# Optimization experiments

Measured on AMD Instinct MI355X. Metric: run time of the kernel, lower is better.

Reference implementation:

```python
import jax, jax.numpy as jnp
import numpy as np

EMBED = 1024
HEADS = 16
HEAD_DIM = EMBED // HEADS
FFN = 4096
BSZ = 2
CHUNK = 128
NCHUNK = 16
REG_LEN = CHUNK * NCHUNK   # 2048
SUM_LEN = NCHUNK           # 1 summary token per chunk
NEG = -1e9


def _layer_norm(x, g, b, eps=1e-5):
    mu = x.mean(-1, keepdims=True)
    var = ((x - mu) ** 2).mean(-1, keepdims=True)
    return (x - mu) * jax.lax.rsqrt(var + eps) * g + b


def _build_mask(reg_chunk_ranges, sum_len, reg_len):
    # True = attention allowed. Museformer hierarchical scheme:
    #   rr: reg token attends reg tokens of its OWN chunk, causally
    #   rs: reg token attends summary tokens of STRICTLY EARLIER chunks
    #   sr: summary token of chunk c attends reg tokens of chunk c
    #   ss: causal among summary tokens
    bsz = reg_chunk_ranges.shape[0]
    starts = reg_chunk_ranges[:, :, 0]                       # [B, C]
    t = jnp.arange(reg_len)
    chunk_id = (t[None, :, None] >= starts[:, None, :]).sum(-1) - 1   # [B, R]
    sum_chunk = jnp.arange(sum_len)                          # [S]
    rr = (chunk_id[:, :, None] == chunk_id[:, None, :]) & (t[None, :, None] >= t[None, None, :])
    rs = sum_chunk[None, None, :] < chunk_id[:, :, None]     # [B, R, S]
    sr = chunk_id[:, None, :] == sum_chunk[None, :, None]    # [B, S, R]
    ss = jnp.broadcast_to(sum_chunk[:, None] >= sum_chunk[None, :], (bsz, sum_len, sum_len))
    top = jnp.concatenate([ss, sr], axis=2)
    bot = jnp.concatenate([rs, rr], axis=2)
    return jnp.concatenate([top, bot], axis=1)               # [B, S+R, S+R]


def _forward(x, w_q, w_k, w_v, w_o,
             ln_sa_sum_g, ln_sa_sum_b, ln_sa_reg_g, ln_sa_reg_b,
             sum_fc1_w, sum_fc1_b, sum_fc2_w, sum_fc2_b,
             reg_fc1_w, reg_fc1_b, reg_fc2_w, reg_fc2_b,
             ln_f_sum_g, ln_f_sum_b, ln_f_reg_g, ln_f_reg_b,
             reg_chunk_ranges, sum_len, reg_len):
    bsz, total, d = x.shape
    # --- self-attention block (pre-norm, separate LN for sum/reg parts) ---
    hs = _layer_norm(x[:, :sum_len], ln_sa_sum_g, ln_sa_sum_b)
    hr = _layer_norm(x[:, sum_len:], ln_sa_reg_g, ln_sa_reg_b)
    h = jnp.concatenate([hs, hr], axis=1)
    q = (h @ w_q.T).reshape(bsz, total, HEADS, HEAD_DIM)
    k = (h @ w_k.T).reshape(bsz, total, HEADS, HEAD_DIM)
    v = (h @ w_v.T).reshape(bsz, total, HEADS, HEAD_DIM)
    scores = jnp.einsum('bqhd,bkhd->bhqk', q, k) * (HEAD_DIM ** -0.5)
    mask = _build_mask(reg_chunk_ranges, sum_len, reg_len)   # [B, T, T] bool
    scores = jnp.where(mask[:, None], scores, NEG)
    attn = jax.nn.softmax(scores, axis=-1)
    ctx = jnp.einsum('bhqk,bkhd->bqhd', attn, v).reshape(bsz, total, d)
    x = x + ctx @ w_o.T
    # --- FFN block (pre-norm, separate LN/FFN for sum/reg parts) ---
    fs = _layer_norm(x[:, :sum_len], ln_f_sum_g, ln_f_sum_b)
    fs = jax.nn.relu(fs @ sum_fc1_w.T + sum_fc1_b) @ sum_fc2_w.T + sum_fc2_b
    fr = _layer_norm(x[:, sum_len:], ln_f_reg_g, ln_f_reg_b)
    fr = jax.nn.relu(fr @ reg_fc1_w.T + reg_fc1_b) @ reg_fc2_w.T + reg_fc2_b
    return x + jnp.concatenate([fs, fr], axis=1)


def setup_inputs() -> dict:
    key = jax.random.key(0)
    ks = jax.random.split(key, 12)
    s = 0.02
    total = SUM_LEN + REG_LEN
    starts = (np.arange(NCHUNK) * CHUNK).astype(np.int32)
    ranges = np.stack([starts, starts + CHUNK], axis=-1)     # [C, 2]
    reg_chunk_ranges = jnp.asarray(np.broadcast_to(ranges, (BSZ, NCHUNK, 2)).copy())
    d = dict(
        x=jax.random.normal(ks[0], (BSZ, total, EMBED), jnp.float32),
        w_q=jax.random.normal(ks[1], (EMBED, EMBED), jnp.float32) * s,
        w_k=jax.random.normal(ks[2], (EMBED, EMBED), jnp.float32) * s,
        w_v=jax.random.normal(ks[3], (EMBED, EMBED), jnp.float32) * s,
        w_o=jax.random.normal(ks[4], (EMBED, EMBED), jnp.float32) * s,
        ln_sa_sum_g=jnp.ones((EMBED,)), ln_sa_sum_b=jnp.zeros((EMBED,)),
        ln_sa_reg_g=jnp.ones((EMBED,)), ln_sa_reg_b=jnp.zeros((EMBED,)),
        sum_fc1_w=jax.random.normal(ks[5], (FFN, EMBED), jnp.float32) * s,
        sum_fc1_b=jnp.zeros((FFN,)),
        sum_fc2_w=jax.random.normal(ks[6], (EMBED, FFN), jnp.float32) * s,
        sum_fc2_b=jnp.zeros((EMBED,)),
        reg_fc1_w=jax.random.normal(ks[7], (FFN, EMBED), jnp.float32) * s,
        reg_fc1_b=jnp.zeros((FFN,)),
        reg_fc2_w=jax.random.normal(ks[8], (EMBED, FFN), jnp.float32) * s,
        reg_fc2_b=jnp.zeros((EMBED,)),
        ln_f_sum_g=jnp.ones((EMBED,)), ln_f_sum_b=jnp.zeros((EMBED,)),
        ln_f_reg_g=jnp.ones((EMBED,)), ln_f_reg_b=jnp.zeros((EMBED,)),
        reg_chunk_ranges=reg_chunk_ranges,
        sum_len=SUM_LEN,
        reg_len=REG_LEN,
    )
    return d


def reference(x, w_q, w_k, w_v, w_o,
              ln_sa_sum_g, ln_sa_sum_b, ln_sa_reg_g, ln_sa_reg_b,
              sum_fc1_w, sum_fc1_b, sum_fc2_w, sum_fc2_b,
              reg_fc1_w, reg_fc1_b, reg_fc2_w, reg_fc2_b,
              ln_f_sum_g, ln_f_sum_b, ln_f_reg_g, ln_f_reg_b,
              reg_chunk_ranges, sum_len, reg_len):
    return _forward(x, w_q, w_k, w_v, w_o,
                    ln_sa_sum_g, ln_sa_sum_b, ln_sa_reg_g, ln_sa_reg_b,
                    sum_fc1_w, sum_fc1_b, sum_fc2_w, sum_fc2_b,
                    reg_fc1_w, reg_fc1_b, reg_fc2_w, reg_fc2_b,
                    ln_f_sum_g, ln_f_sum_b, ln_f_reg_g, ln_f_reg_b,
                    reg_chunk_ranges, sum_len, reg_len)
```

## Files before the change

### kernel.cpp

```cpp
#include <hip/hip_runtime.h>
#include <stdint.h>

typedef __attribute__((ext_vector_type(8))) short short8;
typedef __attribute__((ext_vector_type(4))) float f32x4;

__device__ __forceinline__ float bf2f(short s) {
    union { unsigned u; float f; } c;
    c.u = ((unsigned)(unsigned short)s) << 16;
    return c.f;
}
__device__ __forceinline__ short f2bf(float f) {
    union { float f; unsigned u; } c; c.f = f;
    unsigned u = c.u + 0x7fffu + ((c.u >> 16) & 1u);
    return (short)(u >> 16);
}
__device__ __forceinline__ void gll16(const short* g, short* l) {
    __builtin_amdgcn_global_load_lds(
        (const __attribute__((address_space(1))) unsigned int*)g,
        (__attribute__((address_space(3))) unsigned int*)l, 16, 0, 0);
}
#define MFMA(a, b, c) __builtin_amdgcn_mfma_f32_16x16x32_bf16((a), (b), (c), 0, 0, 0)

__global__ __launch_bounds__(256) void cvt_w(
    const float* __restrict__ wq, const float* __restrict__ wk,
    const float* __restrict__ wv, const float* __restrict__ wo,
    const float* __restrict__ f1s, const float* __restrict__ f2s,
    const float* __restrict__ f1r, const float* __restrict__ f2r,
    short* __restrict__ dst)
{
    size_t i = ((size_t)blockIdx.x * 256 + threadIdx.x) * 4;
    const float* src; size_t off;
    if (i < 4194304) {
        int seg = (int)(i >> 20);
        src = seg == 0 ? wq : seg == 1 ? wk : seg == 2 ? wv : wo;
        off = i & 1048575;
    } else {
        size_t ii = i - 4194304;
        int seg = (int)(ii >> 22);
        src = seg == 0 ? f1s : seg == 1 ? f2s : seg == 2 ? f1r : f2r;
        off = ii & 4194303;
    }
    float4 v = *(const float4*)(src + off);
    short4 o;
    o.x = f2bf(v.x); o.y = f2bf(v.y); o.z = f2bf(v.z); o.w = f2bf(v.w);
    *(short4*)(dst + i) = o;
}

template<int PHASE>
__global__ __launch_bounds__(256) void ln_k(
    const float* __restrict__ xin, const short* __restrict__ Pw, float* __restrict__ x1out,
    const float* __restrict__ g_sum, const float* __restrict__ b_sum,
    const float* __restrict__ g_reg, const float* __restrict__ b_reg,
    short* __restrict__ out_all, short* __restrict__ out_s, short* __restrict__ out_r)
{
    int row = blockIdx.x;
    int b = row / 2064, t = row - b * 2064;
    int tid = threadIdx.x;
    int c = tid * 4;
    size_t base = (size_t)row * 1024 + c;
    float4 v = *(const float4*)(xin + base);
    if (PHASE == 1) {
#pragma unroll
        for (int z = 0; z < 2; ++z) {
            short4 p = *(const short4*)(Pw + (size_t)z * 4227072 + base);
            v.x += bf2f(p.x); v.y += bf2f(p.y);
            v.z += bf2f(p.z); v.w += bf2f(p.w);
        }
        *(float4*)(x1out + base) = v;
    }
    float s = v.x + v.y + v.z + v.w;
#pragma unroll
    for (int off = 1; off < 64; off <<= 1) s += __shfl_xor(s, off);
    __shared__ float red[8];
    if ((tid & 63) == 0) red[tid >> 6] = s;
    __syncthreads();
    float mu = (red[0] + red[1] + red[2] + red[3]) * (1.0f / 1024.0f);
    float a0 = v.x - mu, a1 = v.y - mu, a2 = v.z - mu, a3 = v.w - mu;
    float qq = a0 * a0 + a1 * a1 + a2 * a2 + a3 * a3;
#pragma unroll
    for (int off = 1; off < 64; off <<= 1) qq += __shfl_xor(qq, off);
    if ((tid & 63) == 0) red[4 + (tid >> 6)] = qq;
    __syncthreads();
    float var = (red[4] + red[5] + red[6] + red[7]) * (1.0f / 1024.0f);
    float rs = rsqrtf(var + 1e-5f);
    const float* g  = (t < 16) ? g_sum : g_reg;
    const float* be = (t < 16) ? b_sum : b_reg;
    short4 o;
    o.x = f2bf(a0 * rs * g[c]     + be[c]);
    o.y = f2bf(a1 * rs * g[c + 1] + be[c + 1]);
    o.z = f2bf(a2 * rs * g[c + 2] + be[c + 2]);
    o.w = f2bf(a3 * rs * g[c + 3] + be[c + 3]);
    short* dst;
    if (PHASE == 0) dst = out_all + (size_t)row * 1024;
    else dst = (t < 16) ? (out_s + ((size_t)b * 16 + t) * 1024)
                        : (out_r + ((size_t)b * 2048 + (t - 16)) * 1024);
    *(short4*)(dst + c) = o;
}

template<int MODE>
__global__ __launch_bounds__(512, 2) void gemm8p(
    const short* __restrict__ A, int M, int K, int klen,
    const short* __restrict__ B0, const short* __restrict__ B1, const short* __restrict__ B2,
    const float* __restrict__ bias,
    void* __restrict__ o0, void* __restrict__ o1, void* __restrict__ o2, int seg)
{
    const int tid = threadIdx.x;
    const int w = tid >> 6, l = tid & 63;
    const int lr = l & 15, lh = l >> 4;
    const int m0 = blockIdx.x * 256;
    int ntile = blockIdx.y, nsel = 0;
    const short* B = B0;
    if (MODE == 0) { nsel = ntile >> 2; ntile &= 3; B = nsel == 0 ? B0 : (nsel == 1 ? B1 : B2); }
    const int n0 = ntile * 256;
    const int wm = w >> 2, wn = w & 3;
    const int kbase = blockIdx.z * klen;

    __shared__ __align__(16) short L[2 * 32768];

    const int srow = tid >> 2;
    const int scb  = (tid & 3) ^ ((srow >> 1) & 3);
    int ar0 = m0 + srow;        if (ar0 > M - 1) ar0 = M - 1;
    int ar1 = m0 + srow + 128;  if (ar1 > M - 1) ar1 = M - 1;
    const short* gA0 = A + (size_t)ar0 * K + kbase + scb * 8;
    const short* gA1 = A + (size_t)ar1 * K + kbase + scb * 8;
    const short* gB0 = B + (size_t)(n0 + srow) * K + kbase + scb * 8;
    const short* gB1 = B + (size_t)(n0 + srow + 128) * K + kbase + scb * 8;
    const int wofs = w * 512;
    const int cbrd = (lh ^ ((lr >> 1) & 3)) * 8;

    f32x4 acc[8][4];
#pragma unroll
    for (int m = 0; m < 8; ++m)
#pragma unroll
        for (int n = 0; n < 4; ++n) acc[m][n] = (f32x4){0.f, 0.f, 0.f, 0.f};

    auto STG = [&](int tt, int s, bool isB) {
        const int off = (tt & 1) * 32768 + s * 16384 + (isB ? 8192 : 0);
        const int gk  = tt * 64 + s * 32;
        if (!isB) {
            gll16(gA0 + gk, L + off + wofs);
            gll16(gA1 + gk, L + off + 4096 + wofs);
        } else {
            gll16(gB0 + gk, L + off + wofs);
            gll16(gB1 + gk, L + off + 4096 + wofs);
        }
    };

    const int nt = klen >> 6;
    STG(0, 0, false); STG(0, 0, true); STG(0, 1, false); STG(0, 1, true);

    const int arow = wm * 128, brow = wn * 64;

    for (int t = 0; t < nt; ++t) {
        const int buf = (t & 1) * 32768;
        const short* LA0 = L + buf;
        const short* LB0 = L + buf + 8192;
        const short* LA1 = L + buf + 16384;
        const short* LB1 = L + buf + 24576;

        asm volatile("s_waitcnt vmcnt(4)" ::: "memory");
        __builtin_amdgcn_s_barrier();
        asm volatile("" ::: "memory");
        if (t + 1 < nt) STG(t + 1, 0, false);
        short8 a0[8];
#pragma unroll
        for (int m = 0; m < 8; ++m)
            a0[m] = *(const short8*)(LA0 + (arow + m * 16 + lr) * 32 + cbrd);
        short8 b0 = *(const short8*)(LB0 + (brow + lr) * 32 + cbrd);
        short8 b1 = *(const short8*)(LB0 + (brow + 16 + lr) * 32 + cbrd);
        __builtin_amdgcn_s_setprio(1);
#pragma unroll
        for (int m = 0; m < 8; ++m) {
            acc[m][0] = MFMA(a0[m], b0, acc[m][0]);
            acc[m][1] = MFMA(a0[m], b1, acc[m][1]);
        }
        __builtin_amdgcn_s_setprio(0);

        if (t + 1 < nt) asm volatile("s_waitcnt vmcnt(2)" ::: "memory");
        else            asm volatile("s_waitcnt vmcnt(0)" ::: "memory");
        __builtin_amdgcn_s_barrier();
        asm volatile("" ::: "memory");
        if (t + 1 < nt) STG(t + 1, 0, true);
        short8 b2 = *(const short8*)(LB0 + (brow + 32 + lr) * 32 + cbrd);
        short8 b3 = *(const short8*)(LB0 + (brow + 48 + lr) * 32 + cbrd);
        __builtin_amdgcn_s_setprio(1);
#pragma unroll
        for (int m = 0; m < 8; ++m) {
            acc[m][2] = MFMA(a0[m], b2, acc[m][2]);
            acc[m][3] = MFMA(a0[m], b3, acc[m][3]);
        }
        __builtin_amdgcn_s_setprio(0);
        short8 a1[8];
#pragma unroll
        for (int m = 0; m < 8; ++m)
            a1[m] = *(const short8*)(LA1 + (arow + m * 16 + lr) * 32 + cbrd);
        short8 c0 = *(const short8*)(LB1 + (brow + lr) * 32 + cbrd);
        short8 c1 = *(const short8*)(LB1 + (brow + 16 + lr) * 32 + cbrd);

        __builtin_amdgcn_s_barrier();
        asm volatile("" ::: "memory");
        if (t + 1 < nt) STG(t + 1, 1, false);
        __builtin_amdgcn_s_setprio(1);
#pragma unroll
        for (int m = 0; m < 8; ++m) {
            acc[m][0] = MFMA(a1[m], c0, acc[m][0]);
            acc[m][1] = MFMA(a1[m], c1, acc[m][1]);
        }
        __builtin_amdgcn_s_setprio(0);
        short8 c2 = *(const short8*)(LB1 + (brow + 32 + lr) * 32 + cbrd);
        short8 c3 = *(const short8*)(LB1 + (brow + 48 + lr) * 32 + cbrd);

        __builtin_amdgcn_s_barrier();
        asm volatile("" ::: "memory");
        if (t + 1 < nt) STG(t + 1, 1, true);
        __builtin_amdgcn_s_setprio(1);
#pragma unroll
        for (int m = 0; m < 8; ++m) {
            acc[m][2] = MFMA(a1[m], c2, acc[m][2]);
            acc[m][3] = MFMA(a1[m], c3, acc[m][3]);
        }
        __builtin_amdgcn_s_setprio(0);
    }

#pragma unroll
    for (int m = 0; m < 8; ++m) {
#pragma unroll
        for (int n = 0; n < 4; ++n) {
            int gc = n0 + wn * 64 + n * 16 + lr;
#pragma unroll
            for (int j = 0; j < 4; ++j) {
                int gr = m0 + wm * 128 + m * 16 + lh * 4 + j;
                if (gr >= M) continue;
                float val = acc[m][n][j];
                if (MODE == 0) {
                    short* o = (short*)(nsel == 0 ? o0 : (nsel == 1 ? o1 : o2));
                    o[(size_t)gr * 1024 + gc] = f2bf(val);
                } else if (MODE == 2) {
                    val += bias[gc];
                    val = val > 0.f ? val : 0.f;
                    ((short*)o0)[(size_t)gr * 4096 + gc] = f2bf(val);
                } else {
                    short* P = (short*)o0 + (size_t)blockIdx.z * (size_t)seg;
                    P[(size_t)gr * 1024 + gc] = f2bf(val);
                }
            }
        }
    }
}

template<int MODE>
__global__ __launch_bounds__(256) void gemm_bt(
    const short* __restrict__ A, int M, int K, int klen,
    const short* __restrict__ B0,
    const float* __restrict__ bias,
    void* __restrict__ o0, int seg)
{
    const int tid = threadIdx.x;
    const int w = tid >> 6, l = tid & 63;
    const int lr = l & 15, lh = l >> 4;
    const int m0 = blockIdx.x * 128;
    const int n0 = blockIdx.y * 128;
    const short* B = B0;
    const int wr = (w >> 1) * 64, wc = (w & 1) * 64;
    const int kbase = blockIdx.z * klen;

    __shared__ __align__(16) short As[2 * 4096];
    __shared__ __align__(16) short Bs[2 * 4096];

    const int srow = w * 32 + (l >> 2);
    const int scol = (((l & 3) ^ ((l >> 3) & 3))) * 8;
    int ar0 = m0 + srow;      if (ar0 > M - 1) ar0 = M - 1;
    int ar1 = m0 + srow + 16; if (ar1 > M - 1) ar1 = M - 1;
    const short* ga0 = A + (size_t)ar0 * K + scol + kbase;
    const short* ga1 = A + (size_t)ar1 * K + scol + kbase;
    const short* gb0 = B + (size_t)(n0 + srow) * K + scol + kbase;
    const short* gb1 = B + (size_t)(n0 + srow + 16) * K + scol + kbase;
    const int lofs = (w * 32) * 32;
    const int cbrd = (lh ^ ((lr >> 1) & 3)) * 8;

    f32x4 acc[4][4];
#pragma unroll
    for (int m = 0; m < 4; ++m)
#pragma unroll
        for (int n = 0; n < 4; ++n) acc[m][n] = (f32x4){0.f, 0.f, 0.f, 0.f};

    auto STAGE = [&](int j, int buf) {
        const int k0 = j * 32;
        short* a = As + buf * 4096 + lofs;
        short* b = Bs + buf * 4096 + lofs;
        gll16(ga0 + k0, a);
        gll16(ga1 + k0, a + 512);
        gll16(gb0 + k0, b);
        gll16(gb1 + k0, b + 512);
    };

    const int nk = klen >> 5;
    STAGE(0, 0);
    for (int t = 0; t < nk; ++t) {
        __syncthreads();
        const int cur = (t & 1);
        if (t + 1 < nk) STAGE(t + 1, cur ^ 1);
        const int co = cur << 12;
        short8 af[4], bfr[4];
#pragma unroll
        for (int m = 0; m < 4; ++m)
            af[m] = *(const short8*)(As + co + (wr + m * 16 + lr) * 32 + cbrd);
#pragma unroll
        for (int n = 0; n < 4; ++n)
            bfr[n] = *(const short8*)(Bs + co + (wc + n * 16 + lr) * 32 + cbrd);
#pragma unroll
        for (int m = 0; m < 4; ++m)
#pragma unroll
            for (int n = 0; n < 4; ++n)
                acc[m][n] = MFMA(af[m], bfr[n], acc[m][n]);
    }

#pragma unroll
    for (int m = 0; m < 4; ++m) {
#pragma unroll
        for (int n = 0; n < 4; ++n) {
            int gc = n0 + wc + n * 16 + lr;
#pragma unroll
            for (int j = 0; j < 4; ++j) {
                int gr = m0 + wr + m * 16 + lh * 4 + j;
                if (gr >= M) continue;
                float val = acc[m][n][j];
                if (MODE == 1) {
                    float* P = (float*)o0 + (size_t)blockIdx.z * (size_t)seg;
                    P[(size_t)gr * 1024 + gc] = val;
                } else {
                    val += bias[gc];
                    val = val > 0.f ? val : 0.f;
                    ((short*)o0)[(size_t)gr * 4096 + gc] = f2bf(val);
                }
            }
        }
    }
}

__global__ __launch_bounds__(256) void reduce_f2reg(
    const float* __restrict__ x1, const short* __restrict__ P,
    const float* __restrict__ bias, float* __restrict__ out)
{
    size_t i = ((size_t)blockIdx.x * 256 + threadIdx.x) * 4;
    int gr = (int)(i >> 10), c = (int)(i & 1023);
    size_t g = (size_t)((gr >> 11) * 2064 + 16 + (gr & 2047)) * 1024 + c;
    float4 r  = *(const float4*)(x1 + g);
    float4 bb = *(const float4*)(bias + c);
    float ox = r.x + bb.x, oy = r.y + bb.y, oz = r.z + bb.z, ow = r.w + bb.w;
#pragma unroll
    for (int z = 0; z < 4; ++z) {
        short4 p = *(const short4*)(P + (size_t)z * 4194304 + i);
        ox += bf2f(p.x); oy += bf2f(p.y); oz += bf2f(p.z); ow += bf2f(p.w);
    }
    float4 o; o.x = ox; o.y = oy; o.z = oz; o.w = ow;
    *(float4*)(out + g) = o;
}

__global__ __launch_bounds__(256) void reduce_f2sum(
    const float* __restrict__ x1, const float* __restrict__ P,
    const float* __restrict__ bias, float* __restrict__ out)
{
    int i = (blockIdx.x * 256 + threadIdx.x) * 4;
    int gr = i >> 10, c = i & 1023;
    size_t g = (size_t)((gr >> 4) * 2064 + (gr & 15)) * 1024 + c;
    float4 r  = *(const float4*)(x1 + g);
    float4 bb = *(const float4*)(bias + c);
    float ox = r.x + bb.x, oy = r.y + bb.y, oz = r.z + bb.z, ow = r.w + bb.w;
#pragma unroll
    for (int s = 0; s < 16; ++s) {
        float4 p = *(const float4*)(P + s * 32768 + i);
        ox += p.x; oy += p.y; oz += p.z; ow += p.w;
    }
    float4 o; o.x = ox; o.y = oy; o.z = oz; o.w = ow;
    *(float4*)(out + g) = o;
}

__global__ __launch_bounds__(256) void attn_reg(
    const short* __restrict__ q, const short* __restrict__ k,
    const short* __restrict__ v, short* __restrict__ ctx)
{
    __shared__ __align__(16) short Pl[128 * 168];
    __shared__ __align__(16) short Vt[64 * 168];
    short* Kl = Pl;

    const int tid = threadIdx.x;
    const int w = tid >> 6, l = tid & 63, lr = l & 15, lh = l >> 4;
    const int c = blockIdx.x, h = blockIdx.y, b = blockIdx.z;
    const int hc = h * 64;
    const size_t rowq0 = (size_t)b * 2064 + 16 + (size_t)c * 128;

    for (int ch = tid; ch < 1152; ch += 256) {
        int row = ch >> 3, kk = (ch & 7) << 3;
        size_t grow = (row < 16) ? ((size_t)b * 2064 + row) : (rowq0 + row - 16);
        *(int4*)(Kl + row * 72 + kk) = *(const int4*)(k + grow * 1024 + hc + kk);
    }
    for (int ch = tid; ch < 1152; ch += 256) {
        int j = ch % 144, db = ch / 144;
        size_t grow = (j < 16) ? ((size_t)b * 2064 + j) : (rowq0 + j - 16);
        short8 dv = *(const short8*)(v + grow * 1024 + hc + db * 8);
#pragma unroll
        for (int i = 0; i < 8; ++i) Vt[(db * 8 + i) * 168 + j] = dv[i];
    }
    for (int idx = tid; idx < 1024; idx += 256) {
        int d = idx >> 4, jj = 144 + (idx & 15);
        Vt[d * 168 + jj] = 0;
    }
    __syncthreads();

    short8 qf[2][2];
#pragma unroll
    for (int m = 0; m < 2; ++m) {
        size_t grow = rowq0 + w * 32 + m * 16 + lr;
#pragma unroll
        for (int ks = 0; ks < 2; ++ks)
            qf[m][ks] = *(const short8*)(q + grow * 1024 + hc + ks * 32 + lh * 8);
    }

    f32x4 s[2][9];
#pragma unroll
    for (int m = 0; m < 2; ++m)
#pragma unroll
        for (int n = 0; n < 9; ++n) s[m][n] = (f32x4){0.f, 0.f, 0.f, 0.f};
    __builtin_amdgcn_s_setprio(1);
#pragma unroll
    for (int n = 0; n < 9; ++n) {
        const short* kr = Kl + (n * 16 + lr) * 72;
        short8 k0 = *(const short8*)(kr + lh * 8);
        short8 k1 = *(const short8*)(kr + 32 + lh * 8);
        s[0][n] = MFMA(qf[0][0], k0, s[0][n]);
        s[0][n] = MFMA(qf[0][1], k1, s[0][n]);
        s[1][n] = MFMA(qf[1][0], k0, s[1][n]);
        s[1][n] = MFMA(qf[1][1], k1, s[1][n]);
    }
    __builtin_amdgcn_s_setprio(0);

    float inv_[2][4];
#pragma unroll
    for (int m = 0; m < 2; ++m) {
#pragma unroll
        for (int j = 0; j < 4; ++j) {
            int p = w * 32 + m * 16 + lh * 4 + j;
            float best = -1e30f;
            float e[9];
#pragma unroll
            for (int n = 0; n < 9; ++n) {
                int kk = n * 16 + lr;
                bool vis = (kk < 16) ? (kk < c) : (kk - 16 <= p);
                float val = vis ? s[m][n][j] * 0.125f : -1e30f;
                e[n] = val;
                best = fmaxf(best, val);
            }
#pragma unroll
            for (int off = 1; off < 16; off <<= 1) best = fmaxf(best, __shfl_xor(best, off));
            float sm = 0.f;
#pragma unroll
            for (int n = 0; n < 9; ++n) {
                float ex = __expf(e[n] - best);
                s[m][n][j] = ex;
                sm += ex;
            }
#pragma unroll
            for (int off = 1; off < 16; off <<= 1) sm += __shfl_xor(sm, off);
            inv_[m][j] = 1.0f / sm;
        }
    }

    __syncthreads();
#pragma unroll
    for (int m = 0; m < 2; ++m)
#pragma unroll
        for (int n = 0; n < 9; ++n)
#pragma unroll
            for (int j = 0; j < 4; ++j)
                Pl[(w * 32 + m * 16 + lh * 4 + j) * 168 + n * 16 + lr] = f2bf(s[m][n][j]);
    for (int idx = l; idx < 512; idx += 64) {
        int rr = idx >> 4, kkp = 144 + (idx & 15);
        Pl[(w * 32 + rr) * 168 + kkp] = 0;
    }
    __syncthreads();

    f32x4 dacc[2][4];
#pragma unroll
    for (int m = 0; m < 2; ++m)
#pragma unroll
        for (int n = 0; n < 4; ++n) dacc[m][n] = (f32x4){0.f, 0.f, 0.f, 0.f};
#pragma unroll
    for (int ks = 0; ks < 5; ++ks) {
        int kk0 = ks * 32;
        short8 pa[2];
#pragma unroll
        for (int m = 0; m < 2; ++m)
            pa[m] = *(const short8*)(Pl + (w * 32 + m * 16 + lr) * 168 + kk0 + lh * 8);
        __builtin_amdgcn_s_setprio(1);
#pragma unroll
        for (int n = 0; n < 4; ++n) {
            short8 vb = *(const short8*)(Vt + (n * 16 + lr) * 168 + kk0 + lh * 8);
            dacc[0][n] = MFMA(pa[0], vb, dacc[0][n]);
            dacc[1][n] = MFMA(pa[1], vb, dacc[1][n]);
        }
        __builtin_amdgcn_s_setprio(0);
    }

#pragma unroll
    for (int m = 0; m < 2; ++m)
#pragma unroll
        for (int n = 0; n < 4; ++n)
#pragma unroll
            for (int j = 0; j < 4; ++j) {
                int p = w * 32 + m * 16 + lh * 4 + j;
                ctx[(rowq0 + p) * 1024 + hc + n * 16 + lr] = f2bf(dacc[m][n][j] * inv_[m][j]);
            }
}

__global__ __launch_bounds__(64) void attn_sum(
    const short* __restrict__ q, const short* __restrict__ k,
    const short* __restrict__ v, short* __restrict__ ctx)
{
    int idx = blockIdx.x;
    int b = idx >> 8, h = (idx >> 4) & 15, s = idx & 15;
    int l = threadIdx.x;
    int hc = h * 64;
    size_t qrow = (size_t)b * 2064 + s;
    __shared__ float qv[64];
    __shared__ float pp[192];
    qv[l] = bf2f(q[qrow * 1024 + hc + l]);
    __syncthreads();
    float sc[3];
#pragma unroll
    for (int i = 0; i < 3; ++i) {
        int j = l + i * 64;
        float t = -1e30f;
        if (j < 144 && (j >= 16 || j <= s)) {
            size_t kr = (j < 16) ? ((size_t)b * 2064 + j)
                                 : ((size_t)b * 2064 + 16 + (size_t)s * 128 + (j - 16));
            const short* kp = k + kr * 1024 + hc;
            float acc = 0.f;
            for (int d = 0; d < 64; ++d) acc += qv[d] * bf2f(kp[d]);
            t = acc * 0.125f;
        }
        sc[i] = t;
    }
    float mx = fmaxf(sc[0], fmaxf(sc[1], sc[2]));
#pragma unroll
    for (int off = 1; off < 64; off <<= 1) mx = fmaxf(mx, __shfl_xor(mx, off));
    float sm = 0.f;
#pragma unroll
    for (int i = 0; i < 3; ++i) {
        float ex = (sc[i] > -1e29f) ? __expf(sc[i] - mx) : 0.f;
        pp[l + i * 64] = ex;
        sm += ex;
    }
#pragma unroll
    for (int off = 1; off < 64; off <<= 1) sm += __shfl_xor(sm, off);
    __syncthreads();
    float invs = 1.0f / sm;
    float acc = 0.f;
    for (int j = 0; j < 144; ++j) {
        float pj = pp[j];
        size_t vr = (j < 16) ? ((size_t)b * 2064 + j)
                             : ((size_t)b * 2064 + 16 + (size_t)s * 128 + (j - 16));
        acc += pj * bf2f(v[vr * 1024 + hc + l]);
    }
    ctx[qrow * 1024 + hc + l] = f2bf(acc * invs);
}

extern "C" void kernel_launch(void* const* d_in, const int* in_sizes, int n_in,
                              void* d_out, int out_size, void* d_ws, size_t ws_size,
                              hipStream_t stream) {
    const float* x    = (const float*)d_in[0];
    const float* wq   = (const float*)d_in[1];
    const float* wk   = (const float*)d_in[2];
    const float* wv   = (const float*)d_in[3];
    const float* wo   = (const float*)d_in[4];
    const float* lsg  = (const float*)d_in[5];
    const float* lsb  = (const float*)d_in[6];
    const float* lrg  = (const float*)d_in[7];
    const float* lrb  = (const float*)d_in[8];
    const float* sf1w = (const float*)d_in[9];
    const float* sf1b = (const float*)d_in[10];
    const float* sf2w = (const float*)d_in[11];
    const float* sf2b = (const float*)d_in[12];
    const float* rf1w = (const float*)d_in[13];
    const float* rf1b = (const float*)d_in[14];
    const float* rf2w = (const float*)d_in[15];
    const float* rf2b = (const float*)d_in[16];
    const float* fsg  = (const float*)d_in[17];
    const float* fsb  = (const float*)d_in[18];
    const float* frg  = (const float*)d_in[19];
    const float* frb  = (const float*)d_in[20];
    float* out = (float*)d_out;

    char* ws = (char*)d_ws;
    short* wbf   = (short*)ws;
    short* wq_b  = wbf;
    short* wk_b  = wbf + 1048576;
    short* wv_b  = wbf + 2097152;
    short* wo_b  = wbf + 3145728;
    short* f1s_b = wbf + 4194304;
    short* f2s_b = wbf + 8388608;
    short* f1r_b = wbf + 12582912;
    short* f2r_b = wbf + 16777216;
    short* h_all = (short*)(ws + 41943040);
    short* qb   = (short*)(ws + 50397184);
    short* kb   = qb + 4227072;
    short* vb   = kb + 4227072;
    short* ctxb = vb + 4227072;
    short* Pwo  = (short*)(ws + 41943040);
    float* x1   = (float*)(ws + 84213760);
    short* h2_reg = (short*)ws;
    short* h2_sum = (short*)(ws + 75759616);
    short* f1_reg = (short*)(ws + 41943040);
    short* f1_sum = (short*)(ws + 75825152);
    float* Psum   = (float*)(ws + 8388608);
    short* Pf2    = (short*)ws;

    cvt_w<<<20480, 256, 0, stream>>>(wq, wk, wv, wo, sf1w, sf2w, rf1w, rf2w, wbf);
    ln_k<0><<<4128, 256, 0, stream>>>(x, nullptr, nullptr, lsg, lsb, lrg, lrb,
                                      h_all, nullptr, nullptr);
    gemm8p<0><<<dim3(17, 12, 1), 512, 0, stream>>>(h_all, 4128, 1024, 1024,
        wq_b, wk_b, wv_b, nullptr, qb, kb, vb, 0);
    attn_reg<<<dim3(16, 16, 2), 256, 0, stream>>>(qb, kb, vb, ctxb);
    attn_sum<<<512, 64, 0, stream>>>(qb, kb, vb, ctxb);
    gemm8p<3><<<dim3(17, 4, 2), 512, 0, stream>>>(ctxb, 4128, 1024, 512,
        wo_b, nullptr, nullptr, nullptr, Pwo, nullptr, nullptr, 4227072);
    ln_k<1><<<4128, 256, 0, stream>>>(x, Pwo, x1, fsg, fsb, frg, frb,
                                      nullptr, h2_sum, h2_reg);
    gemm8p<2><<<dim3(16, 16, 1), 512, 0, stream>>>(h2_reg, 4096, 1024, 1024,
        f1r_b, nullptr, nullptr, rf1b, f1_reg, nullptr, nullptr, 0);
    gemm_bt<2><<<dim3(1, 32, 1), 256, 0, stream>>>(h2_sum, 32, 1024, 1024,
        f1s_b, sf1b, f1_sum, 0);
    gemm_bt<1><<<dim3(1, 8, 16), 256, 0, stream>>>(f1_sum, 32, 4096, 256,
        f2s_b, nullptr, Psum, 32768);
    reduce_f2sum<<<32, 256, 0, stream>>>(x1, Psum, sf2b, out);
    gemm8p<3><<<dim3(16, 4, 4), 512, 0, stream>>>(f1_reg, 4096, 4096, 1024,
        f2r_b, nullptr, nullptr, nullptr, Pf2, nullptr, nullptr, 4194304);
    reduce_f2reg<<<4096, 256, 0, stream>>>(x1, Pf2, rf2b, out);
}
```

Before: 277.2 us.

## Add 256x128-tile GEMM variant for QKV and output projections

Result: slower. 290.2 us (+4.7%).

```diff
diff --git a/kernel.cpp b/kernel.cpp
--- a/kernel.cpp
+++ b/kernel.cpp
@@ -239,6 +239,151 @@
                     val += bias[gc];
                     val = val > 0.f ? val : 0.f;
                     ((short*)o0)[(size_t)gr * 4096 + gc] = f2bf(val);
+                } else {
+                    short* P = (short*)o0 + (size_t)blockIdx.z * (size_t)seg;
+                    P[(size_t)gr * 1024 + gc] = f2bf(val);
+                }
+            }
+        }
+    }
+}
+
+template<int MODE>
+__global__ __launch_bounds__(512, 2) void gemm4q(
+    const short* __restrict__ A, int M, int K, int klen,
+    const short* __restrict__ B0, const short* __restrict__ B1, const short* __restrict__ B2,
+    void* __restrict__ o0, void* __restrict__ o1, void* __restrict__ o2, int seg)
+{
+    const int tid = threadIdx.x;
+    const int w = tid >> 6, l = tid & 63;
+    const int lr = l & 15, lh = l >> 4;
+    const int m0 = blockIdx.x * 256;
+    int ntile = blockIdx.y, nsel = 0;
+    const short* B = B0;
+    if (MODE == 0) { nsel = ntile >> 3; ntile &= 7; B = nsel == 0 ? B0 : (nsel == 1 ? B1 : B2); }
+    const int n0 = ntile * 128;
+    const int wm = w >> 1, wn = w & 1;
+    const int kbase = blockIdx.z * klen;
+
+    __shared__ __align__(16) short L[2 * 24576];
+
+    const int srow = tid >> 2;
+    const int scb  = (tid & 3) ^ ((srow >> 1) & 3);
+    int ar0 = m0 + srow;        if (ar0 > M - 1) ar0 = M - 1;
+    int ar1 = m0 + srow + 128;  if (ar1 > M - 1) ar1 = M - 1;
+    const short* gA0 = A + (size_t)ar0 * K + kbase + scb * 8;
+    const short* gA1 = A + (size_t)ar1 * K + kbase + scb * 8;
+    const short* gB0 = B + (size_t)(n0 + srow) * K + kbase + scb * 8;
+    const int wofs = w * 512;
+    const int cbrd = (lh ^ ((lr >> 1) & 3)) * 8;
+
+    f32x4 acc[4][4];
+#pragma unroll
+    for (int m = 0; m < 4; ++m)
+#pragma unroll
+        for (int n = 0; n < 4; ++n) acc[m][n] = (f32x4){0.f, 0.f, 0.f, 0.f};
+
+    auto STGA = [&](int tt, int s) {
+        const int off = (tt & 1) * 24576 + s * 12288;
+        const int gk  = tt * 64 + s * 32;
+        gll16(gA0 + gk, L + off + wofs);
+        gll16(gA1 + gk, L + off + 4096 + wofs);
+    };
+    auto STGB = [&](int tt, int s) {
+        const int off = (tt & 1) * 24576 + s * 12288 + 8192;
+        const int gk  = tt * 64 + s * 32;
+        gll16(gB0 + gk, L + off + wofs);
+    };
+
+    const int nt = klen >> 6;
+    STGA(0, 0); STGB(0, 0); STGA(0, 1); STGB(0, 1);
+
+    const int arow = wm * 64, brow = wn * 64;
+
+    for (int t = 0; t < nt; ++t) {
+        const int buf = (t & 1) * 24576;
+        const short* LA0 = L + buf;
+        const short* LB0 = L + buf + 8192;
+        const short* LA1 = L + buf + 12288;
+        const short* LB1 = L + buf + 20480;
+
+        asm volatile("s_waitcnt vmcnt(3)" ::: "memory");
+        __builtin_amdgcn_s_barrier();
+        asm volatile("" ::: "memory");
+        if (t + 1 < nt) STGA(t + 1, 0);
+        short8 a0[4];
+#pragma unroll
+        for (int m = 0; m < 4; ++m)
+            a0[m] = *(const short8*)(LA0 + (arow + m * 16 + lr) * 32 + cbrd);
+        short8 b0 = *(const short8*)(LB0 + (brow + lr) * 32 + cbrd);
+        short8 b1 = *(const short8*)(LB0 + (brow + 16 + lr) * 32 + cbrd);
+        __builtin_amdgcn_s_setprio(1);
+#pragma unroll
+        for (int m = 0; m < 4; ++m) {
+            acc[m][0] = MFMA(a0[m], b0, acc[m][0]);
+            acc[m][1] = MFMA(a0[m], b1, acc[m][1]);
+        }
+        __builtin_amdgcn_s_setprio(0);
+
+        if (t + 1 < nt) asm volatile("s_waitcnt vmcnt(2)" ::: "memory");
+        else            asm volatile("s_waitcnt vmcnt(0)" ::: "memory");
+        __builtin_amdgcn_s_barrier();
+        asm volatile("" ::: "memory");
+        if (t + 1 < nt) STGB(t + 1, 0);
+        short8 b2 = *(const short8*)(LB0 + (brow + 32 + lr) * 32 + cbrd);
+        short8 b3 = *(const short8*)(LB0 + (brow + 48 + lr) * 32 + cbrd);
+        __builtin_amdgcn_s_setprio(1);
+#pragma unroll
+        for (int m = 0; m < 4; ++m) {
+            acc[m][2] = MFMA(a0[m], b2, acc[m][2]);
+            acc[m][3] = MFMA(a0[m], b3, acc[m][3]);
+        }
+        __builtin_amdgcn_s_setprio(0);
+        short8 a1[4];
+#pragma unroll
+        for (int m = 0; m < 4; ++m)
+            a1[m] = *(const short8*)(LA1 + (arow + m * 16 + lr) * 32 + cbrd);
+        short8 c0 = *(const short8*)(LB1 + (brow + lr) * 32 + cbrd);
+        short8 c1 = *(const short8*)(LB1 + (brow + 16 + lr) * 32 + cbrd);
+
+        __builtin_amdgcn_s_barrier();
+        asm volatile("" ::: "memory");
+        if (t + 1 < nt) STGA(t + 1, 1);
+        __builtin_amdgcn_s_setprio(1);
+#pragma unroll
+        for (int m = 0; m < 4; ++m) {
+            acc[m][0] = MFMA(a1[m], c0, acc[m][0]);
+            acc[m][1] = MFMA(a1[m], c1, acc[m][1]);
+        }
+        __builtin_amdgcn_s_setprio(0);
+        short8 c2 = *(const short8*)(LB1 + (brow + 32 + lr) * 32 + cbrd);
+        short8 c3 = *(const short8*)(LB1 + (brow + 48 + lr) * 32 + cbrd);
+
+        __builtin_amdgcn_s_barrier();
+        asm volatile("" ::: "memory");
+        if (t + 1 < nt) STGB(t + 1, 1);
+        __builtin_amdgcn_s_setprio(1);
+#pragma unroll
+        for (int m = 0; m < 4; ++m) {
+            acc[m][2] = MFMA(a1[m], c2, acc[m][2]);
+            acc[m][3] = MFMA(a1[m], c3, acc[m][3]);
+        }
+        __builtin_amdgcn_s_setprio(0);
+    }
+
+#pragma unroll
+    for (int m = 0; m < 4; ++m) {
+#pragma unroll
+        for (int n = 0; n < 4; ++n) {
+            int gc = n0 + wn * 64 + n * 16 + lr;
+#pragma unroll
+            for (int j = 0; j < 4; ++j) {
+                int gr = m0 + wm * 64 + m * 16 + lh * 4 + j;
+                if (gr >= M) continue;
+                float val = acc[m][n][j];
+                if (MODE == 0) {
+                    short* o = (short*)(nsel == 0 ? o0 : (nsel == 1 ? o1 : o2));
+                    o[(size_t)gr * 1024 + gc] = f2bf(val);
                 } else {
                     short* P = (short*)o0 + (size_t)blockIdx.z * (size_t)seg;
                     P[(size_t)gr * 1024 + gc] = f2bf(val);
@@ -618,12 +763,12 @@
     cvt_w<<<20480, 256, 0, stream>>>(wq, wk, wv, wo, sf1w, sf2w, rf1w, rf2w, wbf);
     ln_k<0><<<4128, 256, 0, stream>>>(x, nullptr, nullptr, lsg, lsb, lrg, lrb,
                                       h_all, nullptr, nullptr);
-    gemm8p<0><<<dim3(17, 12, 1), 512, 0, stream>>>(h_all, 4128, 1024, 1024,
-        wq_b, wk_b, wv_b, nullptr, qb, kb, vb, 0);
+    gemm4q<0><<<dim3(17, 24, 1), 512, 0, stream>>>(h_all, 4128, 1024, 1024,
+        wq_b, wk_b, wv_b, qb, kb, vb, 0);
     attn_reg<<<dim3(16, 16, 2), 256, 0, stream>>>(qb, kb, vb, ctxb);
     attn_sum<<<512, 64, 0, stream>>>(qb, kb, vb, ctxb);
-    gemm8p<3><<<dim3(17, 4, 2), 512, 0, stream>>>(ctxb, 4128, 1024, 512,
-        wo_b, nullptr, nullptr, nullptr, Pwo, nullptr, nullptr, 4227072);
+    gemm4q<3><<<dim3(17, 8, 2), 512, 0, stream>>>(ctxb, 4128, 1024, 512,
+        wo_b, nullptr, nullptr, Pwo, nullptr, nullptr, 4227072);
     ln_k<1><<<4128, 256, 0, stream>>>(x, Pwo, x1, fsg, fsb, frg, frb,
                                       nullptr, h2_sum, h2_reg);
     gemm8p<2><<<dim3(16, 16, 1), 512, 0, stream>>>(h2_reg, 4096, 1024, 1024,
```
